# Kernel optimization log

Measured on AMD Instinct MI355X. Metric: run time of the kernel, lower is better.

## Reference

```python
import jax, jax.numpy as jnp
import numpy as np

TOP_K = 2


def setup_inputs() -> dict:
    key = jax.random.key(0)
    kx, kw = jax.random.split(key)
    B, S, D, E = 4, 4096, 2048, 64
    x = jax.random.normal(kx, (B, S, D), dtype=jnp.float32)
    W = jax.random.normal(kw, (E, D), dtype=jnp.float32) * 0.02  # router weight [E, D]
    return {"x": x, "W": W}


def reference(x, W):
    B, S, D = x.shape
    E = W.shape[0]
    x_flat = x.reshape(-1, D)                      # [T, D], T = B*S
    router_logits = jnp.einsum('td,ed->te', x_flat, W)  # [T, E]
    router_probs = jax.nn.softmax(router_logits, axis=-1)
    expert_weights, expert_indices = jax.lax.top_k(router_probs, TOP_K)  # [T, K]
    expert_weights = expert_weights / jnp.sum(expert_weights, axis=-1, keepdims=True)
    expert_indices = expert_indices.reshape(B, S, TOP_K)
    expert_weights = expert_weights.reshape(B, S, TOP_K)
    # aux load-balance loss: sum((mean usage - 1/E)^2)
    expert_usage = jnp.mean(router_probs, axis=0)  # [E]
    aux_loss = jnp.sum((expert_usage - 1.0 / E) ** 2)
    return expert_indices, expert_weights, aux_loss
```

## Files before the change

### kernel.cpp

```cpp
#include <hip/hip_runtime.h>
#include <math.h>

#define T_TOK 16384
#define DDIM  2048
#define NE    64
#define NPLANE (NE * DDIM)
#define NBLK  512

typedef __attribute__((ext_vector_type(8))) short short8;
typedef __attribute__((ext_vector_type(4))) float floatx4;

union Frag8 { unsigned short u[8]; short8 v; };

__device__ __forceinline__ unsigned int bf16_rne_bits(float x) {
    unsigned int u = __builtin_bit_cast(unsigned int, x);
    return (u + 0x7fffu + ((u >> 16) & 1u)) & 0xffff0000u;
}

__device__ __forceinline__ void dma16(const float* g, float* lds) {
    __builtin_amdgcn_global_load_lds(
        (const __attribute__((address_space(1))) unsigned int*)g,
        (__attribute__((address_space(3))) unsigned int*)lds, 16, 0, 0);
}

__global__ void wsplit_kernel(const float* __restrict__ W,
                              unsigned short* __restrict__ wh,
                              unsigned short* __restrict__ wm,
                              unsigned short* __restrict__ wl) {
    int i  = blockIdx.x * 256 + threadIdx.x;
    int j  = i & 7;
    int cl = (i >> 3) & 15;
    int q  = (i >> 7) & 3;
    int et = (i >> 9) & 3;
    int kc = i >> 11;
    int e  = et * 16 + cl;
    int k  = kc * 32 + q * 8 + j;
    float w = W[e * DDIM + k];
    unsigned int hb = bf16_rne_bits(w);
    float r  = w - __builtin_bit_cast(float, hb);
    unsigned int mb = bf16_rne_bits(r);
    float r2 = r - __builtin_bit_cast(float, mb);
    unsigned int lb = bf16_rne_bits(r2);
    wh[i] = (unsigned short)(hb >> 16);
    wm[i] = (unsigned short)(mb >> 16);
    wl[i] = (unsigned short)(lb >> 16);
}

__global__ __launch_bounds__(1024, 8)
void router_main(const float* __restrict__ x,
                 const unsigned short* __restrict__ wh,
                 const unsigned short* __restrict__ wm,
                 const unsigned short* __restrict__ wl,
                 float* __restrict__ out, float* __restrict__ usage_part) {
    __shared__ float As[2 * 8192];
    __shared__ float ured[16][NE];
    float* lg = As;

    const int tid  = threadIdx.x;
    const int lane = tid & 63;
    const int wv   = __builtin_amdgcn_readfirstlane(tid >> 6);
    const int nh   = wv & 1;
    const int kq   = wv >> 1;
    const int cl   = lane & 15;
    const int q    = lane >> 4;
    const int t0   = blockIdx.x * 32;

    const int tlA0 = 2 * wv, tlA1 = 2 * wv + 1;
    const float* ax0 = x + (size_t)(t0 + tlA0) * DDIM + ((lane ^ (tlA0 & 7)) << 2);
    const float* ax1 = x + (size_t)(t0 + tlA1) * DDIM + ((lane ^ (tlA1 & 7)) << 2);

    floatx4 acc[2][2];
#pragma unroll
    for (int mt = 0; mt < 2; ++mt)
#pragma unroll
        for (int nt = 0; nt < 2; ++nt)
            acc[mt][nt] = (floatx4){0.f, 0.f, 0.f, 0.f};

    const unsigned lofs   = (unsigned)((q * 16 + cl) << 3);
    const unsigned bfrag0 = ((unsigned)(kq * 4 + nh * 2 + 0) << 9) + lofs;
    const unsigned bfrag1 = ((unsigned)(kq * 4 + nh * 2 + 1) << 9) + lofs;

    dma16(ax0, As + tlA0 * 256);
    dma16(ax1, As + tlA1 * 256);

#pragma unroll 1
    for (int c = 0; c < 8; ++c) {
        __syncthreads();

        if (c + 1 < 8) {
            float* nb = As + ((c + 1) & 1) * 8192;
            dma16(ax0 + (c + 1) * 256, nb + tlA0 * 256);
            dma16(ax1 + (c + 1) * 256, nb + tlA1 * 256);
        }

        const unsigned bo = (unsigned)c * 16384u;
        uint4 cb[2][3];
        {
            const unsigned o0 = bo + bfrag0, o1 = bo + bfrag1;
            cb[0][0] = *(const uint4*)(wh + o0);
            cb[0][1] = *(const uint4*)(wm + o0);
            cb[0][2] = *(const uint4*)(wl + o0);
            cb[1][0] = *(const uint4*)(wh + o1);
            cb[1][1] = *(const uint4*)(wm + o1);
            cb[1][2] = *(const uint4*)(wl + o1);
        }

        const float* buf = As + (c & 1) * 8192;
        const int h0 = (kq * 8 + q * 2) ^ (cl & 7);
        short8 Ah[2], Am[2], Al[2];
#pragma unroll
        for (int mt = 0; mt < 2; ++mt) {
            const float* ap = buf + (mt * 16 + cl) * 256;
            float4 a0 = *(const float4*)(ap + h0 * 4);
            float4 a1 = *(const float4*)(ap + (h0 ^ 1) * 4);
            float f[8] = {a0.x, a0.y, a0.z, a0.w, a1.x, a1.y, a1.z, a1.w};
            Frag8 fh, fm, fl;
#pragma unroll
            for (int j = 0; j < 8; ++j) {
                unsigned int ub = __builtin_bit_cast(unsigned int, f[j]);
                unsigned int hb = ub & 0xffff0000u;
                float r = f[j] - __builtin_bit_cast(float, hb);
                unsigned int rb = __builtin_bit_cast(unsigned int, r);
                unsigned int mb = rb & 0xffff0000u;
                float r2 = r - __builtin_bit_cast(float, mb);
                unsigned int lb = __builtin_bit_cast(unsigned int, r2);
                fh.u[j] = (unsigned short)(hb >> 16);
                fm.u[j] = (unsigned short)(mb >> 16);
                fl.u[j] = (unsigned short)(lb >> 16);
            }
            Ah[mt] = fh.v; Am[mt] = fm.v; Al[mt] = fl.v;
        }

#pragma unroll
        for (int mt = 0; mt < 2; ++mt)
#pragma unroll
            for (int nt = 0; nt < 2; ++nt) {
                short8 Bh = __builtin_bit_cast(short8, cb[nt][0]);
                short8 Bm = __builtin_bit_cast(short8, cb[nt][1]);
                short8 Bl = __builtin_bit_cast(short8, cb[nt][2]);
                floatx4 a = acc[mt][nt];
                a = __builtin_amdgcn_mfma_f32_16x16x32_bf16(Ah[mt], Bh, a, 0, 0, 0);
                a = __builtin_amdgcn_mfma_f32_16x16x32_bf16(Ah[mt], Bm, a, 0, 0, 0);
                a = __builtin_amdgcn_mfma_f32_16x16x32_bf16(Am[mt], Bh, a, 0, 0, 0);
                a = __builtin_amdgcn_mfma_f32_16x16x32_bf16(Am[mt], Bm, a, 0, 0, 0);
                a = __builtin_amdgcn_mfma_f32_16x16x32_bf16(Ah[mt], Bl, a, 0, 0, 0);
                a = __builtin_amdgcn_mfma_f32_16x16x32_bf16(Al[mt], Bh, a, 0, 0, 0);
                acc[mt][nt] = a;
            }
    }

    __syncthreads();

#pragma unroll
    for (int mt = 0; mt < 2; ++mt)
#pragma unroll
        for (int nt = 0; nt < 2; ++nt)
#pragma unroll
            for (int r = 0; r < 4; ++r)
                lg[kq * 2048 + (mt * 16 + q * 4 + r) * 64 + nh * 32 + nt * 16 + cl]
                    = acc[mt][nt][r];
    __syncthreads();

    float usage_acc = 0.f;
#pragma unroll 1
    for (int j = 0; j < 2; ++j) {
        const int tl = wv * 2 + j;
        const int t  = t0 + tl;
        float l = (((lg[0 * 2048 + tl * 64 + lane] + lg[1 * 2048 + tl * 64 + lane]) +
                    (lg[2 * 2048 + tl * 64 + lane] + lg[3 * 2048 + tl * 64 + lane])) +
                   ((lg[4 * 2048 + tl * 64 + lane] + lg[5 * 2048 + tl * 64 + lane]) +
                    (lg[6 * 2048 + tl * 64 + lane] + lg[7 * 2048 + tl * 64 + lane])));

        float v1 = l; int i1 = lane;
#pragma unroll
        for (int off = 32; off >= 1; off >>= 1) {
            float ov = __shfl_xor(v1, off, 64);
            int   oi = __shfl_xor(i1, off, 64);
            if (ov > v1 || (ov == v1 && oi < i1)) { v1 = ov; i1 = oi; }
        }
        float lm = (lane == i1) ? -INFINITY : l;
        float v2 = lm; int i2 = lane;
#pragma unroll
        for (int off = 32; off >= 1; off >>= 1) {
            float ov = __shfl_xor(v2, off, 64);
            int   oi = __shfl_xor(i2, off, 64);
            if (ov > v2 || (ov == v2 && oi < i2)) { v2 = ov; i2 = oi; }
        }

        float p = expf(l - v1);
        float s = p;
#pragma unroll
        for (int off = 32; off >= 1; off >>= 1) s += __shfl_xor(s, off, 64);

        float e2  = expf(v2 - v1);
        float rcp = 1.0f / (1.0f + e2);
        usage_acc += p / s;

        if (lane == 0) {
            out[(size_t)t * 2 + 0]         = (float)i1;
            out[(size_t)t * 2 + 1]         = (float)i2;
            out[32768 + (size_t)t * 2 + 0] = rcp;
            out[32768 + (size_t)t * 2 + 1] = e2 * rcp;
        }
    }

    ured[wv][lane] = usage_acc;
    __syncthreads();
    if (wv == 0) {
        float s = (((ured[0][lane] + ured[1][lane]) + (ured[2][lane] + ured[3][lane])) +
                   ((ured[4][lane] + ured[5][lane]) + (ured[6][lane] + ured[7][lane]))) +
                  (((ured[8][lane] + ured[9][lane]) + (ured[10][lane] + ured[11][lane])) +
                   ((ured[12][lane] + ured[13][lane]) + (ured[14][lane] + ured[15][lane])));
        usage_part[(size_t)blockIdx.x * 64 + lane] = s;
    }
}

__global__ __launch_bounds__(1024)
void router_aux(const float* __restrict__ usage_part, float* __restrict__ out) {
    __shared__ float red[16][NE];
    const int tid = threadIdx.x;
    const int e   = tid & 63;
    const int g   = tid >> 6;
    float s = 0.f;
#pragma unroll
    for (int i = 0; i < NBLK / 16; ++i)
        s += usage_part[(size_t)(g * (NBLK / 16) + i) * 64 + e];
    red[g][e] = s;
    __syncthreads();
    if (g == 0) {
        float tot = 0.f;
#pragma unroll
        for (int i = 0; i < 16; ++i) tot += red[i][e];
        float u = tot * (1.0f / 16384.0f) - (1.0f / 64.0f);
        float sq = u * u;
#pragma unroll
        for (int off = 32; off >= 1; off >>= 1) sq += __shfl_xor(sq, off, 64);
        if (e == 0) out[65536] = sq;
    }
}

extern "C" void kernel_launch(void* const* d_in, const int* in_sizes, int n_in,
                              void* d_out, int out_size, void* d_ws, size_t ws_size,
                              hipStream_t stream) {
    const float* x = (const float*)d_in[0];
    const float* W = (const float*)d_in[1];
    float* out     = (float*)d_out;

    unsigned short* ws_h = (unsigned short*)d_ws;
    unsigned short* ws_m = ws_h + NPLANE;
    unsigned short* ws_l = ws_m + NPLANE;
    float* upart         = (float*)(ws_l + NPLANE);

    wsplit_kernel<<<dim3(NPLANE / 256), dim3(256), 0, stream>>>(W, ws_h, ws_m, ws_l);
    router_main<<<dim3(NBLK), dim3(1024), 0, stream>>>(x, ws_h, ws_m, ws_l, out, upart);
    router_aux<<<dim3(1), dim3(1024), 0, stream>>>(upart, out);
}
```

Baseline: 232.6 us.

## Split-K router GEMM into single-wave blocks with separate reduction kernel

Replaces the 1024-thread block kernel with a split-K scheme. Each 64-thread block computes a 32-token by 64-expert partial over one eighth of K, reading x straight from global memory into registers with a one-step prefetch. The partials go to workspace, and a second kernel sums them and does softmax, top-2 and usage. This drops LDS staging and block-wide barriers in favour of many small independent blocks, at the cost of an extra 32 MB round trip for partials and an additional launch. The old path is kept as a fallback when the workspace is too small.

Result: no change. 229.4 us (-1.4%).

```diff
diff --git a/kernel.cpp b/kernel.cpp
--- a/kernel.cpp
+++ b/kernel.cpp
@@ -6,6 +6,7 @@
 #define NE    64
 #define NPLANE (NE * DDIM)
 #define NBLK  512
+#define KSPLIT 8
 
 typedef __attribute__((ext_vector_type(8))) short short8;
 typedef __attribute__((ext_vector_type(4))) float floatx4;
@@ -46,74 +47,45 @@
     wl[i] = (unsigned short)(lb >> 16);
 }
 
-__global__ __launch_bounds__(1024, 8)
-void router_main(const float* __restrict__ x,
-                 const unsigned short* __restrict__ wh,
-                 const unsigned short* __restrict__ wm,
-                 const unsigned short* __restrict__ wl,
-                 float* __restrict__ out, float* __restrict__ usage_part) {
-    __shared__ float As[2 * 8192];
-    __shared__ float ured[16][NE];
-    float* lg = As;
-
-    const int tid  = threadIdx.x;
-    const int lane = tid & 63;
-    const int wv   = __builtin_amdgcn_readfirstlane(tid >> 6);
-    const int nh   = wv & 1;
-    const int kq   = wv >> 1;
+__global__ __launch_bounds__(64, 4)
+void router_partial(const float* __restrict__ x,
+                    const unsigned short* __restrict__ wh,
+                    const unsigned short* __restrict__ wm,
+                    const unsigned short* __restrict__ wl,
+                    float* __restrict__ part) {
+    const int lane = threadIdx.x;
+    const int b    = blockIdx.x;
+    const int kq   = b & 7;
+    const int tb   = b >> 3;
     const int cl   = lane & 15;
     const int q    = lane >> 4;
-    const int t0   = blockIdx.x * 32;
-
-    const int tlA0 = 2 * wv, tlA1 = 2 * wv + 1;
-    const float* ax0 = x + (size_t)(t0 + tlA0) * DDIM + ((lane ^ (tlA0 & 7)) << 2);
-    const float* ax1 = x + (size_t)(t0 + tlA1) * DDIM + ((lane ^ (tlA1 & 7)) << 2);
-
-    floatx4 acc[2][2];
+    const int t0   = tb * 32;
+
+    const float* xa = x + (size_t)(t0 + cl) * DDIM + kq * 256 + q * 8;
+    const unsigned lofs = (unsigned)((q * 16 + cl) << 3);
+
+    floatx4 acc[2][4];
 #pragma unroll
     for (int mt = 0; mt < 2; ++mt)
 #pragma unroll
-        for (int nt = 0; nt < 2; ++nt)
+        for (int nt = 0; nt < 4; ++nt)
             acc[mt][nt] = (floatx4){0.f, 0.f, 0.f, 0.f};
 
-    const unsigned lofs   = (unsigned)((q * 16 + cl) << 3);
-    const unsigned bfrag0 = ((unsigned)(kq * 4 + nh * 2 + 0) << 9) + lofs;
-    const unsigned bfrag1 = ((unsigned)(kq * 4 + nh * 2 + 1) << 9) + lofs;
-
-    dma16(ax0, As + tlA0 * 256);
-    dma16(ax1, As + tlA1 * 256);
+    float4 a0[2], a1[2];
+#pragma unroll
+    for (int mt = 0; mt < 2; ++mt) {
+        const float* ap = xa + (size_t)mt * 16 * DDIM;
+        a0[mt] = *(const float4*)(ap);
+        a1[mt] = *(const float4*)(ap + 4);
+    }
 
 #pragma unroll 1
-    for (int c = 0; c < 8; ++c) {
-        __syncthreads();
-
-        if (c + 1 < 8) {
-            float* nb = As + ((c + 1) & 1) * 8192;
-            dma16(ax0 + (c + 1) * 256, nb + tlA0 * 256);
-            dma16(ax1 + (c + 1) * 256, nb + tlA1 * 256);
-        }
-
-        const unsigned bo = (unsigned)c * 16384u;
-        uint4 cb[2][3];
-        {
-            const unsigned o0 = bo + bfrag0, o1 = bo + bfrag1;
-            cb[0][0] = *(const uint4*)(wh + o0);
-            cb[0][1] = *(const uint4*)(wm + o0);
-            cb[0][2] = *(const uint4*)(wl + o0);
-            cb[1][0] = *(const uint4*)(wh + o1);
-            cb[1][1] = *(const uint4*)(wm + o1);
-            cb[1][2] = *(const uint4*)(wl + o1);
-        }
-
-        const float* buf = As + (c & 1) * 8192;
-        const int h0 = (kq * 8 + q * 2) ^ (cl & 7);
+    for (int s = 0; s < 8; ++s) {
         short8 Ah[2], Am[2], Al[2];
 #pragma unroll
         for (int mt = 0; mt < 2; ++mt) {
-            const float* ap = buf + (mt * 16 + cl) * 256;
-            float4 a0 = *(const float4*)(ap + h0 * 4);
-            float4 a1 = *(const float4*)(ap + (h0 ^ 1) * 4);
-            float f[8] = {a0.x, a0.y, a0.z, a0.w, a1.x, a1.y, a1.z, a1.w};
+            float f[8] = {a0[mt].x, a0[mt].y, a0[mt].z, a0[mt].w,
+                          a1[mt].x, a1[mt].y, a1[mt].z, a1[mt].w};
             Frag8 fh, fm, fl;
 #pragma unroll
             for (int j = 0; j < 8; ++j) {
@@ -131,6 +103,186 @@
             Ah[mt] = fh.v; Am[mt] = fm.v; Al[mt] = fl.v;
         }
 
+        if (s + 1 < 8) {
+#pragma unroll
+            for (int mt = 0; mt < 2; ++mt) {
+                const float* ap = xa + (size_t)mt * 16 * DDIM + (s + 1) * 32;
+                a0[mt] = *(const float4*)(ap);
+                a1[mt] = *(const float4*)(ap + 4);
+            }
+        }
+
+        const unsigned kc = (unsigned)(kq * 8 + s);
+#pragma unroll
+        for (int nt = 0; nt < 4; ++nt) {
+            const unsigned o = (kc * 16u + (unsigned)nt * 4u) * 128u + lofs;
+            short8 Bh = __builtin_bit_cast(short8, *(const uint4*)(wh + o));
+            short8 Bm = __builtin_bit_cast(short8, *(const uint4*)(wm + o));
+            short8 Bl = __builtin_bit_cast(short8, *(const uint4*)(wl + o));
+#pragma unroll
+            for (int mt = 0; mt < 2; ++mt) {
+                floatx4 a = acc[mt][nt];
+                a = __builtin_amdgcn_mfma_f32_16x16x32_bf16(Ah[mt], Bh, a, 0, 0, 0);
+                a = __builtin_amdgcn_mfma_f32_16x16x32_bf16(Ah[mt], Bm, a, 0, 0, 0);
+                a = __builtin_amdgcn_mfma_f32_16x16x32_bf16(Am[mt], Bh, a, 0, 0, 0);
+                a = __builtin_amdgcn_mfma_f32_16x16x32_bf16(Am[mt], Bm, a, 0, 0, 0);
+                a = __builtin_amdgcn_mfma_f32_16x16x32_bf16(Ah[mt], Bl, a, 0, 0, 0);
+                a = __builtin_amdgcn_mfma_f32_16x16x32_bf16(Al[mt], Bh, a, 0, 0, 0);
+                acc[mt][nt] = a;
+            }
+        }
+    }
+
+    float* pb = part + ((size_t)kq * T_TOK + (size_t)t0) * NE;
+#pragma unroll
+    for (int mt = 0; mt < 2; ++mt)
+#pragma unroll
+        for (int nt = 0; nt < 4; ++nt)
+#pragma unroll
+            for (int r = 0; r < 4; ++r)
+                pb[(mt * 16 + q * 4 + r) * NE + nt * 16 + cl] = acc[mt][nt][r];
+}
+
+__global__ __launch_bounds__(256)
+void router_reduce(const float* __restrict__ part, float* __restrict__ out,
+                   float* __restrict__ usage_part) {
+    __shared__ float ured[4][NE];
+    const int tid  = threadIdx.x;
+    const int lane = tid & 63;
+    const int wv   = tid >> 6;
+    const int t0   = blockIdx.x * 32;
+    const size_t ps = (size_t)T_TOK * NE;
+
+    float usage_acc = 0.f;
+#pragma unroll 1
+    for (int j = 0; j < 8; ++j) {
+        const int t = t0 + wv * 8 + j;
+        const float* pp = part + (size_t)t * NE + lane;
+        float l = (((pp[0 * ps] + pp[1 * ps]) + (pp[2 * ps] + pp[3 * ps])) +
+                   ((pp[4 * ps] + pp[5 * ps]) + (pp[6 * ps] + pp[7 * ps])));
+
+        float v1 = l; int i1 = lane;
+#pragma unroll
+        for (int off = 32; off >= 1; off >>= 1) {
+            float ov = __shfl_xor(v1, off, 64);
+            int   oi = __shfl_xor(i1, off, 64);
+            if (ov > v1 || (ov == v1 && oi < i1)) { v1 = ov; i1 = oi; }
+        }
+        float lm = (lane == i1) ? -INFINITY : l;
+        float v2 = lm; int i2 = lane;
+#pragma unroll
+        for (int off = 32; off >= 1; off >>= 1) {
+            float ov = __shfl_xor(v2, off, 64);
+            int   oi = __shfl_xor(i2, off, 64);
+            if (ov > v2 || (ov == v2 && oi < i2)) { v2 = ov; i2 = oi; }
+        }
+
+        float p = expf(l - v1);
+        float s = p;
+#pragma unroll
+        for (int off = 32; off >= 1; off >>= 1) s += __shfl_xor(s, off, 64);
+
+        float e2  = expf(v2 - v1);
+        float rcp = 1.0f / (1.0f + e2);
+        usage_acc += p / s;
+
+        if (lane == 0) {
+            out[(size_t)t * 2 + 0]         = (float)i1;
+            out[(size_t)t * 2 + 1]         = (float)i2;
+            out[32768 + (size_t)t * 2 + 0] = rcp;
+            out[32768 + (size_t)t * 2 + 1] = e2 * rcp;
+        }
+    }
+
+    ured[wv][lane] = usage_acc;
+    __syncthreads();
+    if (wv == 0) {
+        float s = (ured[0][lane] + ured[1][lane]) + (ured[2][lane] + ured[3][lane]);
+        usage_part[(size_t)blockIdx.x * 64 + lane] = s;
+    }
+}
+
+__global__ __launch_bounds__(1024, 8)
+void router_main_fb(const float* __restrict__ x,
+                    const unsigned short* __restrict__ wh,
+                    const unsigned short* __restrict__ wm,
+                    const unsigned short* __restrict__ wl,
+                    float* __restrict__ out, float* __restrict__ usage_part) {
+    __shared__ float As[2 * 8192];
+    __shared__ float ured[16][NE];
+    float* lg = As;
+
+    const int tid  = threadIdx.x;
+    const int lane = tid & 63;
+    const int wv   = __builtin_amdgcn_readfirstlane(tid >> 6);
+    const int nh   = wv & 1;
+    const int kq   = wv >> 1;
+    const int cl   = lane & 15;
+    const int q    = lane >> 4;
+    const int t0   = blockIdx.x * 32;
+
+    const int tlA0 = 2 * wv, tlA1 = 2 * wv + 1;
+    const float* ax0 = x + (size_t)(t0 + tlA0) * DDIM + ((lane ^ (tlA0 & 7)) << 2);
+    const float* ax1 = x + (size_t)(t0 + tlA1) * DDIM + ((lane ^ (tlA1 & 7)) << 2);
+
+    floatx4 acc[2][2];
+#pragma unroll
+    for (int mt = 0; mt < 2; ++mt)
+#pragma unroll
+        for (int nt = 0; nt < 2; ++nt)
+            acc[mt][nt] = (floatx4){0.f, 0.f, 0.f, 0.f};
+
+    const unsigned lofs   = (unsigned)((q * 16 + cl) << 3);
+    const unsigned bfrag0 = ((unsigned)(kq * 4 + nh * 2 + 0) << 9) + lofs;
+    const unsigned bfrag1 = ((unsigned)(kq * 4 + nh * 2 + 1) << 9) + lofs;
+
+    dma16(ax0, As + tlA0 * 256);
+    dma16(ax1, As + tlA1 * 256);
+
+#pragma unroll 1
+    for (int c = 0; c < 8; ++c) {
+        __syncthreads();
+        if (c + 1 < 8) {
+            float* nb = As + ((c + 1) & 1) * 8192;
+            dma16(ax0 + (c + 1) * 256, nb + tlA0 * 256);
+            dma16(ax1 + (c + 1) * 256, nb + tlA1 * 256);
+        }
+        const unsigned bo = (unsigned)c * 16384u;
+        uint4 cb[2][3];
+        {
+            const unsigned o0 = bo + bfrag0, o1 = bo + bfrag1;
+            cb[0][0] = *(const uint4*)(wh + o0);
+            cb[0][1] = *(const uint4*)(wm + o0);
+            cb[0][2] = *(const uint4*)(wl + o0);
+            cb[1][0] = *(const uint4*)(wh + o1);
+            cb[1][1] = *(const uint4*)(wm + o1);
+            cb[1][2] = *(const uint4*)(wl + o1);
+        }
+        const float* buf = As + (c & 1) * 8192;
+        const int h0 = (kq * 8 + q * 2) ^ (cl & 7);
+        short8 Ah[2], Am[2], Al[2];
+#pragma unroll
+        for (int mt = 0; mt < 2; ++mt) {
+            const float* ap = buf + (mt * 16 + cl) * 256;
+            float4 a0 = *(const float4*)(ap + h0 * 4);
+            float4 a1 = *(const float4*)(ap + (h0 ^ 1) * 4);
+            float f[8] = {a0.x, a0.y, a0.z, a0.w, a1.x, a1.y, a1.z, a1.w};
+            Frag8 fh, fm, fl;
+#pragma unroll
+            for (int j = 0; j < 8; ++j) {
+                unsigned int ub = __builtin_bit_cast(unsigned int, f[j]);
+                unsigned int hb = ub & 0xffff0000u;
+                float r = f[j] - __builtin_bit_cast(float, hb);
+                unsigned int rb = __builtin_bit_cast(unsigned int, r);
+                unsigned int mb = rb & 0xffff0000u;
+                float r2 = r - __builtin_bit_cast(float, mb);
+                unsigned int lb = __builtin_bit_cast(unsigned int, r2);
+                fh.u[j] = (unsigned short)(hb >> 16);
+                fm.u[j] = (unsigned short)(mb >> 16);
+                fl.u[j] = (unsigned short)(lb >> 16);
+            }
+            Ah[mt] = fh.v; Am[mt] = fm.v; Al[mt] = fl.v;
+        }
 #pragma unroll
         for (int mt = 0; mt < 2; ++mt)
 #pragma unroll
@@ -150,7 +302,6 @@
     }
 
     __syncthreads();
-
 #pragma unroll
     for (int mt = 0; mt < 2; ++mt)
 #pragma unroll
@@ -249,9 +400,25 @@
     unsigned short* ws_h = (unsigned short*)d_ws;
     unsigned short* ws_m = ws_h + NPLANE;
     unsigned short* ws_l = ws_m + NPLANE;
-    float* upart         = (float*)(ws_l + NPLANE);
+    char* ws_tail        = (char*)(ws_l + NPLANE);
+
+    const size_t part_bytes = (size_t)KSPLIT * T_TOK * NE * sizeof(float);
+    const size_t need = 3 * (size_t)NPLANE * sizeof(unsigned short)
+                      + part_bytes + (size_t)NBLK * NE * sizeof(float);
 
     wsplit_kernel<<<dim3(NPLANE / 256), dim3(256), 0, stream>>>(W, ws_h, ws_m, ws_l);
-    router_main<<<dim3(NBLK), dim3(1024), 0, stream>>>(x, ws_h, ws_m, ws_l, out, upart);
-    router_aux<<<dim3(1), dim3(1024), 0, stream>>>(upart, out);
-}
+
+    if (ws_size >= need) {
+        float* part  = (float*)ws_tail;
+        float* upart = part + (size_t)KSPLIT * T_TOK * NE;
+        router_partial<<<dim3(NBLK * KSPLIT), dim3(64), 0, stream>>>(
+            x, ws_h, ws_m, ws_l, part);
+        router_reduce<<<dim3(NBLK), dim3(256), 0, stream>>>(part, out, upart);
+        router_aux<<<dim3(1), dim3(1024), 0, stream>>>(upart, out);
+    } else {
+        float* upart = (float*)ws_tail;
+        router_main_fb<<<dim3(NBLK), dim3(1024), 0, stream>>>(
+            x, ws_h, ws_m, ws_l, out, upart);
+        router_aux<<<dim3(1), dim3(1024), 0, stream>>>(upart, out);
+    }
+}
```
